# Kernel tuning notes

Measured on AMD Instinct MI355X. Metric: run time of the kernel, lower is better.

Reference implementation:

```python
import jax, jax.numpy as jnp
import numpy as np

# ---- static configuration (matches init_kwargs) ----
B = 32
H = 56
W = 56
C = 192
HEADS = 6
WS = 7            # window size
SHIFT = 3         # shift size (WS // 2)
MLP_HIDDEN = 768  # 4 * C
CPB = 256         # clip(56*56//16, 256, 1024)
N = WS * WS       # tokens per window
NW = (H // WS) * (W // WS)  # windows per image
EPS = 1e-5

# ---- static tables (Swin V2 continuous relative position bias) ----
# log-spaced relative coords table: [(2*WS-1)^2, 2]
_r = np.arange(-(WS - 1), WS, dtype=np.float32)
_tab = np.stack(np.meshgrid(_r, _r, indexing='ij'), axis=-1)  # [2WS-1, 2WS-1, 2]
_tab = _tab / (WS - 1) * 8.0  # pretrained_window_size=0 -> use window_size-1
_tab = np.sign(_tab) * np.log2(np.abs(_tab) + 1.0) / np.log2(8.0)
REL_TABLE = jnp.asarray(_tab.reshape(-1, 2))

# relative position index: [N, N] into the (2WS-1)^2 table
_coords = np.stack(np.meshgrid(np.arange(WS), np.arange(WS), indexing='ij'))
_cf = _coords.reshape(2, -1)
_rel = (_cf[:, :, None] - _cf[:, None, :]).transpose(1, 2, 0).astype(np.int64)
_rel[..., 0] += WS - 1
_rel[..., 1] += WS - 1
_rel[..., 0] *= 2 * WS - 1
REL_INDEX = jnp.asarray(_rel.sum(-1))

# shifted-window attention mask: [NW, N, N] with 0 / -100
_img = np.zeros((H, W), dtype=np.float32)
_sl = [slice(0, -WS), slice(-WS, -SHIFT), slice(-SHIFT, None)]
_cnt = 0
for _hs in _sl:
    for _ws in _sl:
        _img[_hs, _ws] = _cnt
        _cnt += 1
_mw = _img.reshape(H // WS, WS, W // WS, WS).transpose(0, 2, 1, 3).reshape(-1, N)
_am = _mw[:, None, :] - _mw[:, :, None]
ATTN_MASK = jnp.asarray(np.where(_am != 0, -100.0, 0.0).astype(np.float32))


def _layer_norm(x, g, b):
    mu = jnp.mean(x, axis=-1, keepdims=True)
    var = jnp.mean(jnp.square(x - mu), axis=-1, keepdims=True)
    return (x - mu) * jax.lax.rsqrt(var + EPS) * g + b


def setup_inputs() -> dict:
    key = jax.random.key(0)
    ks = jax.random.split(key, 10)
    def n(k, shape, s=0.02):
        return jax.random.normal(k, shape, jnp.float32) * s
    return {
        'x': jax.random.normal(ks[0], (B, H * W, C), jnp.float32),
        'qkv_w': n(ks[1], (3 * C, C)),
        'q_bias': jnp.zeros((C,), jnp.float32),
        'v_bias': jnp.zeros((C,), jnp.float32),
        'logit_scale': jnp.full((HEADS, 1, 1), jnp.log(10.0), jnp.float32),
        'cpb_w1': n(ks[2], (CPB, 2)),
        'cpb_b1': jnp.zeros((CPB,), jnp.float32),
        'cpb_w2': n(ks[3], (HEADS, CPB)),
        'proj_w': n(ks[4], (C, C)),
        'proj_b': jnp.zeros((C,), jnp.float32),
        'norm1_g': jnp.ones((C,), jnp.float32),
        'norm1_b': jnp.zeros((C,), jnp.float32),
        'norm2_g': jnp.ones((C,), jnp.float32),
        'norm2_b': jnp.zeros((C,), jnp.float32),
        'fc1_w': n(ks[5], (MLP_HIDDEN, C)),
        'fc1_b': jnp.zeros((MLP_HIDDEN,), jnp.float32),
        'fc2_w': n(ks[6], (C, MLP_HIDDEN)),
        'fc2_b': jnp.zeros((C,), jnp.float32),
    }


def reference(x, qkv_w, q_bias, v_bias, logit_scale, cpb_w1, cpb_b1, cpb_w2,
              proj_w, proj_b, norm1_g, norm1_b, norm2_g, norm2_b,
              fc1_w, fc1_b, fc2_w, fc2_b):
    b = x.shape[0]
    hd = C // HEADS
    shortcut = x

    # cyclic shift + window partition -> [b*NW, N, C]
    xi = jnp.roll(x.reshape(b, H, W, C), (-SHIFT, -SHIFT), axis=(1, 2))
    xw = xi.reshape(b, H // WS, WS, W // WS, WS, C)
    xw = xw.transpose(0, 1, 3, 2, 4, 5).reshape(-1, N, C)

    # qkv projection (k has no bias, per Swin V2)
    qkv_bias = jnp.concatenate([q_bias, jnp.zeros_like(q_bias), v_bias])
    qkv = (xw @ qkv_w.T + qkv_bias).reshape(-1, N, 3, HEADS, hd)
    qkv = qkv.transpose(2, 0, 3, 1, 4)  # [3, bw, heads, N, hd]
    q, k, v = qkv[0], qkv[1], qkv[2]

    # cosine attention with learned logit scale
    q = q / jnp.maximum(jnp.linalg.norm(q, axis=-1, keepdims=True), 1e-12)
    k = k / jnp.maximum(jnp.linalg.norm(k, axis=-1, keepdims=True), 1e-12)
    scale = jnp.exp(jnp.minimum(logit_scale, jnp.log(100.0)))  # [heads,1,1]
    attn = jnp.einsum('bhnd,bhmd->bhnm', q, k) * scale

    # continuous relative position bias via tiny MLP
    tab = jax.nn.relu(REL_TABLE @ cpb_w1.T + cpb_b1) @ cpb_w2.T  # [(2WS-1)^2, heads]
    rpb = 16.0 * jax.nn.sigmoid(tab[REL_INDEX])                  # [N, N, heads]
    attn = attn + rpb.transpose(2, 0, 1)[None]

    # shifted-window mask + softmax
    attn = attn.reshape(-1, NW, HEADS, N, N) + ATTN_MASK[None, :, None]
    attn = jax.nn.softmax(attn.reshape(-1, HEADS, N, N), axis=-1)

    out = jnp.einsum('bhnm,bhmd->bhnd', attn, v)
    out = out.transpose(0, 2, 1, 3).reshape(-1, N, C) @ proj_w.T + proj_b

    # window reverse + reverse shift
    xr = out.reshape(b, H // WS, W // WS, WS, WS, C)
    xr = xr.transpose(0, 1, 3, 2, 4, 5).reshape(b, H, W, C)
    xr = jnp.roll(xr, (SHIFT, SHIFT), axis=(1, 2)).reshape(b, H * W, C)

    # post-norm residual (Swin V2 style)
    x1 = shortcut + _layer_norm(xr, norm1_g, norm1_b)
    hmid = jax.nn.silu(x1 @ fc1_w.T + fc1_b) @ fc2_w.T + fc2_b
    return x1 + _layer_norm(hmid, norm2_g, norm2_b)
```

## Files before the change

kernel.cpp:

```cpp
#include <hip/hip_runtime.h>


typedef unsigned short ushort_t;
using f32x4  = __attribute__((ext_vector_type(4))) float;
using short8 = __attribute__((ext_vector_type(8))) short;
union LD16 { short8 v; ushort4 h[2]; };

__device__ __forceinline__ ushort_t f2bf(float f) {
  union { float f; unsigned u; } v; v.f = f;
  unsigned r = v.u + 0x7fffu + ((v.u >> 16) & 1u);
  return (ushort_t)(r >> 16);
}
__device__ __forceinline__ float bf2f(ushort_t u) {
  union { unsigned u; float f; } v; v.u = ((unsigned)u) << 16;
  return v.f;
}

__device__ __forceinline__ int img_pos(int m) {
  int win = m / 49, n = m - win * 49;
  int b = win >> 6, wi = win & 63;
  int nd = n / 7, nm = n - nd * 7;
  int hs = (wi >> 3) * 7 + nd;
  int ws = (wi & 7) * 7 + nm;
  int h = hs + 3; if (h >= 56) h -= 56;
  int w = ws + 3; if (w >= 56) w -= 56;
  return b * 3136 + h * 56 + w;
}

__device__ __forceinline__ int region3(int a) { return a < 49 ? 0 : (a < 53 ? 1 : 2); }

__global__ void cvt_kernel(const float* __restrict__ in, ushort_t* __restrict__ out, int n) {
  int i = blockIdx.x * 256 + threadIdx.x;
  if (i < n) out[i] = f2bf(in[i]);
}

__global__ __launch_bounds__(256) void gather_cvt_kernel(
    const float* __restrict__ x, ushort_t* __restrict__ xw) {
  int i8 = blockIdx.x * 256 + threadIdx.x;
  int m = i8 / 24, c8 = (i8 - m * 24) * 8;
  const float* p = x + (size_t)img_pos(m) * 192 + c8;
  float4 a = *(const float4*)p, b = *(const float4*)(p + 4);
  ushort_t* q = xw + (size_t)m * 192 + c8;
  *(ushort4*)q       = make_ushort4(f2bf(a.x), f2bf(a.y), f2bf(a.z), f2bf(a.w));
  *(ushort4*)(q + 4) = make_ushort4(f2bf(b.x), f2bf(b.y), f2bf(b.z), f2bf(b.w));
}

__global__ __launch_bounds__(256) void cpb_kernel(
    const float* __restrict__ w1, const float* __restrict__ b1,
    const float* __restrict__ w2, float* __restrict__ tab_s) {
  int e = blockIdx.x;
  int t = threadIdx.x;
  int i = e / 13, j = e - 13 * (e / 13);
  auto cval = [](int a) -> float {
    float r = (a - 6) * (8.0f / 6.0f);
    float v = log2f(fabsf(r) + 1.f) * (1.f / 3.f);
    return r < 0.f ? -v : v;
  };
  float ci = cval(i), cj = cval(j);
  float h = fmaxf(ci * w1[2 * t] + cj * w1[2 * t + 1] + b1[t], 0.f);
  __shared__ float red[256];
  for (int head = 0; head < 6; ++head) {
    red[t] = h * w2[head * 256 + t];
    __syncthreads();
    for (int st = 128; st > 0; st >>= 1) {
      if (t < st) red[t] += red[t + st];
      __syncthreads();
    }
    if (t == 0) tab_s[head * 169 + e] = 16.f / (1.f + __expf(-red[0]));
    __syncthreads();
  }
}

template<int KTOT, int MODE>
__global__ __launch_bounds__(512, 4) void gemm_n192(
    const ushort_t* __restrict__ Ab, const ushort_t* __restrict__ W,
    const float* __restrict__ b0, const float* __restrict__ b1,
    ushort_t* __restrict__ out, int NTOT) {
  __shared__ ushort_t Al[128][40];
  __shared__ ushort_t Bl[192][40];
  int t = threadIdx.x;
  int m0 = blockIdx.x * 128, n0 = blockIdx.y * 192;
  int lane = t & 63, wid = t >> 6;
  int wm = wid >> 1, wn = wid & 1;
  int lr = lane & 15, lg = lane >> 4;

  bool stager = (t < 256);
  int arow = (t & 255) >> 1, akoff = (t & 1) << 4;
  const ushort_t* Arowp = Ab + (size_t)(m0 + arow) * KTOT + akoff;
  int colA = akoff ? 4 : 0;
  int bn = (t & 255) >> 2, cB = t & 3;
  const ushort_t* Browp  = W + (size_t)(n0 + bn) * KTOT + (cB << 3);
  const ushort_t* Browp2 = W + (size_t)(n0 + 64 + bn) * KTOT + (cB << 3);
  const ushort_t* Browp3 = W + (size_t)(n0 + 128 + bn) * KTOT + (cB << 3);
  int colB = ((cB & 1) << 4) | ((cB >> 1) << 2);

  f32x4 acc[2][6];
#pragma unroll
  for (int a = 0; a < 2; ++a)
#pragma unroll
    for (int b = 0; b < 6; ++b) acc[a][b] = (f32x4){0.f, 0.f, 0.f, 0.f};

  LD16 A01, A23, B0, B1, B2;
  auto LOADREGS = [&](int kt) {
    A01.v = *(const short8*)(Arowp + kt);
    A23.v = *(const short8*)(Arowp + kt + 8);
    B0.v  = *(const short8*)(Browp + kt);
    B1.v  = *(const short8*)(Browp2 + kt);
    B2.v  = *(const short8*)(Browp3 + kt);
  };

  const int NT = KTOT / 32;
  if (stager) LOADREGS(0);
  for (int it = 0; it < NT; ++it) {
    if (stager) {
      ushort_t* Ar = &Al[arow][0];
      *(ushort4*)(Ar + colA +  0) = A01.h[0];
      *(ushort4*)(Ar + colA +  8) = A01.h[1];
      *(ushort4*)(Ar + colA + 16) = A23.h[0];
      *(ushort4*)(Ar + colA + 24) = A23.h[1];
      ushort_t* Br0 = &Bl[bn][0];
      *(ushort4*)(Br0 + colB + 0) = B0.h[0];
      *(ushort4*)(Br0 + colB + 8) = B0.h[1];
      ushort_t* Br1 = &Bl[64 + bn][0];
      *(ushort4*)(Br1 + colB + 0) = B1.h[0];
      *(ushort4*)(Br1 + colB + 8) = B1.h[1];
      ushort_t* Br2 = &Bl[128 + bn][0];
      *(ushort4*)(Br2 + colB + 0) = B2.h[0];
      *(ushort4*)(Br2 + colB + 8) = B2.h[1];
    }
    __syncthreads();
    if (stager && it + 1 < NT) LOADREGS((it + 1) * 32);
    short8 af[2], bfv[6];
#pragma unroll
    for (int fm = 0; fm < 2; ++fm)
      af[fm] = *(const short8*)&Al[wm * 32 + fm * 16 + lr][lg * 8];
#pragma unroll
    for (int fn = 0; fn < 6; ++fn)
      bfv[fn] = *(const short8*)&Bl[wn * 96 + fn * 16 + lr][lg * 8];
#pragma unroll
    for (int fm = 0; fm < 2; ++fm)
#pragma unroll
      for (int fn = 0; fn < 6; ++fn)
        acc[fm][fn] = __builtin_amdgcn_mfma_f32_16x16x32_bf16(af[fm], bfv[fn], acc[fm][fn], 0, 0, 0);
    if (it + 1 < NT) __syncthreads();
  }
#pragma unroll
  for (int fm = 0; fm < 2; ++fm) {
#pragma unroll
    for (int fn = 0; fn < 6; ++fn) {
      int col = n0 + wn * 96 + fn * 16 + lr;
      float bias;
      if (MODE == 0) bias = (col < 192) ? b0[col] : ((col < 384) ? 0.f : b1[col - 384]);
      else           bias = b0[col];
#pragma unroll
      for (int r = 0; r < 4; ++r) {
        int row = m0 + wm * 32 + fm * 16 + lg * 4 + r;
        float v = acc[fm][fn][r] + bias;
        if (MODE == 1) v = v / (1.f + __expf(-v));
        out[(size_t)row * NTOT + col] = f2bf(v);
      }
    }
  }
}

template<int KTOT, int MODE>
__global__ __launch_bounds__(512, 4) void gemm_ln512(
    const ushort_t* __restrict__ Ab, const ushort_t* __restrict__ W,
    const float* __restrict__ bias, const float* __restrict__ gamma,
    const float* __restrict__ beta, const float* __restrict__ residf,
    const ushort_t* __restrict__ residb, ushort_t* __restrict__ outb,
    float* __restrict__ outf) {
  __shared__ ushort_t Al[128][40];
  __shared__ ushort_t Bl[192][40];
  int t = threadIdx.x;
  int m0 = blockIdx.x * 128;
  int lane = t & 63, wid = t >> 6;
  int wm = wid >> 1, wn = wid & 1;
  int lr = lane & 15, lg = lane >> 4;

  bool stager = (t < 256);
  int arow = (t & 255) >> 1, akoff = (t & 1) << 4;
  const ushort_t* Arowp = Ab + (size_t)(m0 + arow) * KTOT + akoff;
  int colA = akoff ? 4 : 0;
  int bn = (t & 255) >> 2, cB = t & 3;
  const ushort_t* Browp  = W + (size_t)(bn) * KTOT + (cB << 3);
  const ushort_t* Browp2 = W + (size_t)(64 + bn) * KTOT + (cB << 3);
  const ushort_t* Browp3 = W + (size_t)(128 + bn) * KTOT + (cB << 3);
  int colB = ((cB & 1) << 4) | ((cB >> 1) << 2);

  f32x4 acc[2][6];
#pragma unroll
  for (int a = 0; a < 2; ++a)
#pragma unroll
    for (int b = 0; b < 6; ++b) acc[a][b] = (f32x4){0.f, 0.f, 0.f, 0.f};

  LD16 A01, A23, B0, B1, B2;
  auto LOADREGS = [&](int kt) {
    A01.v = *(const short8*)(Arowp + kt);
    A23.v = *(const short8*)(Arowp + kt + 8);
    B0.v  = *(const short8*)(Browp + kt);
    B1.v  = *(const short8*)(Browp2 + kt);
    B2.v  = *(const short8*)(Browp3 + kt);
  };

  const int NT = KTOT / 32;
  if (stager) LOADREGS(0);
  for (int it = 0; it < NT; ++it) {
    if (stager) {
      ushort_t* Ar = &Al[arow][0];
      *(ushort4*)(Ar + colA +  0) = A01.h[0];
      *(ushort4*)(Ar + colA +  8) = A01.h[1];
      *(ushort4*)(Ar + colA + 16) = A23.h[0];
      *(ushort4*)(Ar + colA + 24) = A23.h[1];
      ushort_t* Br0 = &Bl[bn][0];
      *(ushort4*)(Br0 + colB + 0) = B0.h[0];
      *(ushort4*)(Br0 + colB + 8) = B0.h[1];
      ushort_t* Br1 = &Bl[64 + bn][0];
      *(ushort4*)(Br1 + colB + 0) = B1.h[0];
      *(ushort4*)(Br1 + colB + 8) = B1.h[1];
      ushort_t* Br2 = &Bl[128 + bn][0];
      *(ushort4*)(Br2 + colB + 0) = B2.h[0];
      *(ushort4*)(Br2 + colB + 8) = B2.h[1];
    }
    __syncthreads();
    if (stager && it + 1 < NT) LOADREGS((it + 1) * 32);
    short8 af[2], bfv[6];
#pragma unroll
    for (int fm = 0; fm < 2; ++fm)
      af[fm] = *(const short8*)&Al[wm * 32 + fm * 16 + lr][lg * 8];
#pragma unroll
    for (int fn = 0; fn < 6; ++fn)
      bfv[fn] = *(const short8*)&Bl[wn * 96 + fn * 16 + lr][lg * 8];
#pragma unroll
    for (int fm = 0; fm < 2; ++fm)
#pragma unroll
      for (int fn = 0; fn < 6; ++fn)
        acc[fm][fn] = __builtin_amdgcn_mfma_f32_16x16x32_bf16(af[fm], bfv[fn], acc[fm][fn], 0, 0, 0);
    __syncthreads();
  }

  float* part = (float*)&Bl[0][0];
#pragma unroll
  for (int fm = 0; fm < 2; ++fm) {
#pragma unroll
    for (int r = 0; r < 4; ++r) {
      float s1 = 0.f, s2 = 0.f;
#pragma unroll
      for (int fn = 0; fn < 6; ++fn) {
        int col = wn * 96 + fn * 16 + lr;
        float v = acc[fm][fn][r] + bias[col];
        acc[fm][fn][r] = v;
        s1 += v; s2 += v * v;
      }
#pragma unroll
      for (int off = 1; off < 16; off <<= 1) {
        s1 += __shfl_xor(s1, off);
        s2 += __shfl_xor(s2, off);
      }
      if (lr == 0) {
        int lrow = wm * 32 + fm * 16 + lg * 4 + r;
        part[(wn * 128 + lrow) * 2 + 0] = s1;
        part[(wn * 128 + lrow) * 2 + 1] = s2;
      }
    }
  }
  __syncthreads();
#pragma unroll
  for (int fm = 0; fm < 2; ++fm) {
#pragma unroll
    for (int r = 0; r < 4; ++r) {
      int lrow = wm * 32 + fm * 16 + lg * 4 + r;
      float s1 = part[lrow * 2 + 0] + part[(128 + lrow) * 2 + 0];
      float s2 = part[lrow * 2 + 1] + part[(128 + lrow) * 2 + 1];
      float mean = s1 * (1.f / 192.f);
      float var  = s2 * (1.f / 192.f) - mean * mean;
      float rstd = rsqrtf(fmaxf(var, 0.f) + 1e-5f);
      int rg = m0 + lrow;
      size_t og = (MODE == 0 ? (size_t)img_pos(rg) : (size_t)rg) * 192;
#pragma unroll
      for (int fn = 0; fn < 6; ++fn) {
        int col = wn * 96 + fn * 16 + lr;
        float l = (acc[fm][fn][r] - mean) * rstd * gamma[col] + beta[col];
        if (MODE == 0) outb[og + col] = f2bf(residf[og + col] + l);
        else           outf[og + col] = bf2f(residb[og + col]) + l;
      }
    }
  }
}

__global__ __launch_bounds__(256) void attn_kernel(
    const ushort_t* __restrict__ qkv, const float* __restrict__ logit_scale,
    const float* __restrict__ tab_s, ushort_t* __restrict__ attn_out) {
  __shared__ ushort_t qs[64][40];
  __shared__ ushort_t ksl[64][40];
  __shared__ ushort_t vsl[32][80];
  __shared__ ushort_t ps[64][80];
  __shared__ float tab_l[169];
  int win = blockIdx.x, head = blockIdx.y;
  int t = threadIdx.x;
  int wi = win & 63;
  int wh0 = (wi >> 3) * 7, ww0 = (wi & 7) * 7;
  size_t base = (size_t)win * 49 * 576 + head * 32;

  for (int u = t; u < 169; u += 256) tab_l[u] = tab_s[head * 169 + u];

  for (int u = t; u < 240; u += 256) {
    int arr = u / 120, v = u - arr * 120;
    int r = 49 + (v >> 3), c4 = (v & 7) << 2;
    ushort_t* p = arr ? &ksl[r][c4] : &qs[r][c4];
    *(ushort4*)p = make_ushort4(0, 0, 0, 0);
  }

  for (int u = t; u < 2048; u += 256) {
    int key = u >> 5, d = u & 31;
    ushort_t val = 0;
    if (key < 49) val = qkv[base + (size_t)key * 576 + 384 + d];
    int kk = key & 31;
    int pc = ((key >> 5) << 5) + 8 * ((kk >> 2) & 3) + 4 * (kk >> 4) + (kk & 3);
    vsl[d][pc] = val;
  }

  float scale = __expf(fminf(logit_scale[head], 4.605170186f));

  if (t < 196) {
    int r = t >> 2, c = t & 3;
    const ushort_t* qp = qkv + base + (size_t)r * 576 + c * 8;
    ushort4 qa = *(const ushort4*)qp,         qb = *(const ushort4*)(qp + 4);
    ushort4 ka = *(const ushort4*)(qp + 192), kb = *(const ushort4*)(qp + 196);
    float qf[8] = {bf2f(qa.x), bf2f(qa.y), bf2f(qa.z), bf2f(qa.w),
                   bf2f(qb.x), bf2f(qb.y), bf2f(qb.z), bf2f(qb.w)};
    float kf[8] = {bf2f(ka.x), bf2f(ka.y), bf2f(ka.z), bf2f(ka.w),
                   bf2f(kb.x), bf2f(kb.y), bf2f(kb.z), bf2f(kb.w)};
    float sq = 0.f, sk = 0.f;
#pragma unroll
    for (int d = 0; d < 8; ++d) { sq += qf[d] * qf[d]; sk += kf[d] * kf[d]; }
    sq += __shfl_xor(sq, 1); sq += __shfl_xor(sq, 2);
    sk += __shfl_xor(sk, 1); sk += __shfl_xor(sk, 2);
    float rq = scale / fmaxf(sqrtf(sq), 1e-12f);
    float rk = 1.f   / fmaxf(sqrtf(sk), 1e-12f);
    int c0 = ((c & 1) << 4) | ((c >> 1) << 2);
    ushort_t* qd = &qs[r][c0];
    *(ushort4*)(qd + 0) = make_ushort4(f2bf(qf[0]*rq), f2bf(qf[1]*rq), f2bf(qf[2]*rq), f2bf(qf[3]*rq));
    *(ushort4*)(qd + 8) = make_ushort4(f2bf(qf[4]*rq), f2bf(qf[5]*rq), f2bf(qf[6]*rq), f2bf(qf[7]*rq));
    ushort_t* kd = &ksl[r][c0];
    *(ushort4*)(kd + 0) = make_ushort4(f2bf(kf[0]*rk), f2bf(kf[1]*rk), f2bf(kf[2]*rk), f2bf(kf[3]*rk));
    *(ushort4*)(kd + 8) = make_ushort4(f2bf(kf[4]*rk), f2bf(kf[5]*rk), f2bf(kf[6]*rk), f2bf(kf[7]*rk));
  }
  __syncthreads();

  int lane = t & 63, w = t >> 6;
  int lr = lane & 15, lg = lane >> 4;

  short8 aq = *(const short8*)&qs[w * 16 + lr][lg * 8];
  f32x4 acc[4];
#pragma unroll
  for (int fn = 0; fn < 4; ++fn) {
    acc[fn] = (f32x4){0.f, 0.f, 0.f, 0.f};
    short8 bk = *(const short8*)&ksl[fn * 16 + lr][lg * 8];
    acc[fn] = __builtin_amdgcn_mfma_f32_16x16x32_bf16(aq, bk, acc[fn], 0, 0, 0);
  }

  float rsum[4];
#pragma unroll
  for (int r = 0; r < 4; ++r) {
    int row = w * 16 + lg * 4 + r;
    int rd = (row * 9363) >> 16, rm = row - 7 * rd;
    int gr = region3(wh0 + rd) * 3 + region3(ww0 + rm);
    bool rv = row < 49;
    float sv[4];
#pragma unroll
    for (int fn = 0; fn < 4; ++fn) {
      int col = fn * 16 + lr;
      int jd = (col * 9363) >> 16, jm = col - 7 * jd;
      int gj = region3(wh0 + jd) * 3 + region3(ww0 + jm);
      bool cv = rv && (col < 49);
      int idx = cv ? (rd - jd + 6) * 13 + (rm - jm + 6) : 0;
      float s = acc[fn][r] + tab_l[idx] + (gr == gj ? 0.f : -100.f);
      sv[fn] = cv ? s : -1e30f;
    }
    float m = fmaxf(fmaxf(sv[0], sv[1]), fmaxf(sv[2], sv[3]));
#pragma unroll
    for (int o = 1; o < 16; o <<= 1) m = fmaxf(m, __shfl_xor(m, o));
    float sum = 0.f;
#pragma unroll
    for (int fn = 0; fn < 4; ++fn) {
      float e = __expf(sv[fn] - m);
      sum += e;
      int pc = ((fn >> 1) << 5) + 8 * (lr >> 2) + ((fn & 1) << 2) + (lr & 3);
      ps[row][pc] = f2bf(e);
    }
#pragma unroll
    for (int o = 1; o < 16; o <<= 1) sum += __shfl_xor(sum, o);
    rsum[r] = 1.f / sum;
  }
  __syncthreads();

  short8 ap0 = *(const short8*)&ps[w * 16 + lr][lg * 8];
  short8 ap1 = *(const short8*)&ps[w * 16 + lr][32 + lg * 8];
  f32x4 o2[2];
#pragma unroll
  for (int f = 0; f < 2; ++f) {
    o2[f] = (f32x4){0.f, 0.f, 0.f, 0.f};
    short8 bv0 = *(const short8*)&vsl[f * 16 + lr][lg * 8];
    short8 bv1 = *(const short8*)&vsl[f * 16 + lr][32 + lg * 8];
    o2[f] = __builtin_amdgcn_mfma_f32_16x16x32_bf16(ap0, bv0, o2[f], 0, 0, 0);
    o2[f] = __builtin_amdgcn_mfma_f32_16x16x32_bf16(ap1, bv1, o2[f], 0, 0, 0);
  }
#pragma unroll
  for (int f = 0; f < 2; ++f) {
#pragma unroll
    for (int r = 0; r < 4; ++r) {
      int row = w * 16 + lg * 4 + r;
      if (row < 49)
        attn_out[((size_t)win * 49 + row) * 192 + head * 32 + f * 16 + lr] =
            f2bf(o2[f][r] * rsum[r]);
    }
  }
}

extern "C" void kernel_launch(void* const* d_in, const int* in_sizes, int n_in,
                              void* d_out, int out_size, void* d_ws, size_t ws_size,
                              hipStream_t stream) {
  (void)in_sizes; (void)n_in; (void)out_size; (void)ws_size;
  const float* x    = (const float*)d_in[0];
  const float* qkvw = (const float*)d_in[1];
  const float* qb   = (const float*)d_in[2];
  const float* vb   = (const float*)d_in[3];
  const float* ls   = (const float*)d_in[4];
  const float* cw1  = (const float*)d_in[5];
  const float* cb1  = (const float*)d_in[6];
  const float* cw2  = (const float*)d_in[7];
  const float* pw   = (const float*)d_in[8];
  const float* pb   = (const float*)d_in[9];
  const float* n1g  = (const float*)d_in[10];
  const float* n1b  = (const float*)d_in[11];
  const float* n2g  = (const float*)d_in[12];
  const float* n2b  = (const float*)d_in[13];
  const float* f1w  = (const float*)d_in[14];
  const float* f1b  = (const float*)d_in[15];
  const float* f2w  = (const float*)d_in[16];
  const float* f2b  = (const float*)d_in[17];
  float* out = (float*)d_out;

  char* ws = (char*)d_ws;
  ushort_t* wq_bf = (ushort_t*)ws;
  ushort_t* wp_bf = wq_bf + 110592;
  ushort_t* w1_bf = wp_bf + 36864;
  ushort_t* w2_bf = w1_bf + 147456;
  float*    tab_s = (float*)(w2_bf + 147456);
  const size_t OFF_BIG = 1 << 20;
  ushort_t* qkv_out = (ushort_t*)(ws + OFF_BIG);
  ushort_t* xw_bf   = (ushort_t*)(ws + OFF_BIG + 115605504);
  ushort_t* attn_o  = (ushort_t*)(ws + OFF_BIG + 115605504);
  ushort_t* x1_bf   = (ushort_t*)(ws + OFF_BIG + 154140672);
  ushort_t* hmid    = (ushort_t*)(ws + OFF_BIG);

  cvt_kernel<<<(110592 + 255) / 256, 256, 0, stream>>>(qkvw, wq_bf, 110592);
  cvt_kernel<<<(36864  + 255) / 256, 256, 0, stream>>>(pw,   wp_bf, 36864);
  cvt_kernel<<<(147456 + 255) / 256, 256, 0, stream>>>(f1w,  w1_bf, 147456);
  cvt_kernel<<<(147456 + 255) / 256, 256, 0, stream>>>(f2w,  w2_bf, 147456);
  cpb_kernel<<<169, 256, 0, stream>>>(cw1, cb1, cw2, tab_s);
  gather_cvt_kernel<<<9408, 256, 0, stream>>>(x, xw_bf);

  gemm_n192<192, 0><<<dim3(784, 3), 512, 0, stream>>>(xw_bf, wq_bf, qb, vb, qkv_out, 576);
  attn_kernel<<<dim3(2048, 6), 256, 0, stream>>>(qkv_out, ls, tab_s, attn_o);
  gemm_ln512<192, 0><<<784, 512, 0, stream>>>(attn_o, wp_bf, pb, n1g, n1b, x, nullptr, x1_bf, nullptr);
  gemm_n192<192, 1><<<dim3(784, 4), 512, 0, stream>>>(x1_bf, w1_bf, f1b, nullptr, hmid, 768);
  gemm_ln512<768, 1><<<784, 512, 0, stream>>>(hmid, w2_bf, f2b, n2g, n2b, nullptr, x1_bf, nullptr, out);
}
```

Before: 413.1 us.

## Split projection GEMM from LayerNorm residual into separate kernels

The fused projection GEMM plus LayerNorm epilogue is replaced by a plain GEMM that writes the projection output in place over the attention buffer. A new wave-per-row kernel then does LayerNorm, the shifted-image scatter and the residual add. The fc2 LayerNorm kernel is specialised and drops one redundant barrier on the last K iteration. This removes the cross-wave partial-sum exchange and scattered epilogue from the GEMM, at the cost of an extra full read and write of the activation tensor, plus in-place aliasing that relies on each block owning its rows.

```diff
diff --git a/kernel.cpp b/kernel.cpp
--- a/kernel.cpp
+++ b/kernel.cpp
@@ -75,7 +75,7 @@
 __global__ __launch_bounds__(512, 4) void gemm_n192(
     const ushort_t* __restrict__ Ab, const ushort_t* __restrict__ W,
     const float* __restrict__ b0, const float* __restrict__ b1,
-    ushort_t* __restrict__ out, int NTOT) {
+    ushort_t* out, int NTOT) {
   __shared__ ushort_t Al[128][40];
   __shared__ ushort_t Bl[192][40];
   int t = threadIdx.x;
@@ -163,13 +163,12 @@
   }
 }
 
-template<int KTOT, int MODE>
-__global__ __launch_bounds__(512, 4) void gemm_ln512(
+__global__ __launch_bounds__(512, 4) void gemm_ln_fc2(
     const ushort_t* __restrict__ Ab, const ushort_t* __restrict__ W,
     const float* __restrict__ bias, const float* __restrict__ gamma,
-    const float* __restrict__ beta, const float* __restrict__ residf,
-    const ushort_t* __restrict__ residb, ushort_t* __restrict__ outb,
+    const float* __restrict__ beta, const ushort_t* __restrict__ residb,
     float* __restrict__ outf) {
+  const int KTOT = 768;
   __shared__ ushort_t Al[128][40];
   __shared__ ushort_t Bl[192][40];
   int t = threadIdx.x;
@@ -236,8 +235,9 @@
 #pragma unroll
       for (int fn = 0; fn < 6; ++fn)
         acc[fm][fn] = __builtin_amdgcn_mfma_f32_16x16x32_bf16(af[fm], bfv[fn], acc[fm][fn], 0, 0, 0);
-    __syncthreads();
-  }
+    if (it + 1 < NT) __syncthreads();
+  }
+  __syncthreads();
 
   float* part = (float*)&Bl[0][0];
 #pragma unroll
@@ -275,17 +275,42 @@
       float mean = s1 * (1.f / 192.f);
       float var  = s2 * (1.f / 192.f) - mean * mean;
       float rstd = rsqrtf(fmaxf(var, 0.f) + 1e-5f);
-      int rg = m0 + lrow;
-      size_t og = (MODE == 0 ? (size_t)img_pos(rg) : (size_t)rg) * 192;
+      size_t og = (size_t)(m0 + lrow) * 192;
 #pragma unroll
       for (int fn = 0; fn < 6; ++fn) {
         int col = wn * 96 + fn * 16 + lr;
         float l = (acc[fm][fn][r] - mean) * rstd * gamma[col] + beta[col];
-        if (MODE == 0) outb[og + col] = f2bf(residf[og + col] + l);
-        else           outf[og + col] = bf2f(residb[og + col]) + l;
+        outf[og + col] = bf2f(residb[og + col]) + l;
       }
     }
   }
+}
+
+__global__ __launch_bounds__(256) void ln_resid_kernel(
+    const ushort_t* __restrict__ pre, const float* __restrict__ residf,
+    const float* __restrict__ gamma, const float* __restrict__ beta,
+    ushort_t* __restrict__ outb) {
+  int m = (blockIdx.x * 256 + threadIdx.x) >> 6;
+  int lane = threadIdx.x & 63;
+  const ushort_t* p = pre + (size_t)m * 192;
+  float v0 = bf2f(p[lane]), v1 = bf2f(p[lane + 64]), v2 = bf2f(p[lane + 128]);
+  float s1 = v0 + v1 + v2;
+  float s2 = v0 * v0 + v1 * v1 + v2 * v2;
+#pragma unroll
+  for (int o = 1; o < 64; o <<= 1) {
+    s1 += __shfl_xor(s1, o);
+    s2 += __shfl_xor(s2, o);
+  }
+  float mean = s1 * (1.f / 192.f);
+  float var  = s2 * (1.f / 192.f) - mean * mean;
+  float rstd = rsqrtf(fmaxf(var, 0.f) + 1e-5f);
+  float l0 = (v0 - mean) * rstd * gamma[lane]       + beta[lane];
+  float l1 = (v1 - mean) * rstd * gamma[lane + 64]  + beta[lane + 64];
+  float l2 = (v2 - mean) * rstd * gamma[lane + 128] + beta[lane + 128];
+  size_t og = (size_t)img_pos(m) * 192;
+  outb[og + lane]       = f2bf(residf[og + lane]       + l0);
+  outb[og + lane + 64]  = f2bf(residf[og + lane + 64]  + l1);
+  outb[og + lane + 128] = f2bf(residf[og + lane + 128] + l2);
 }
 
 __global__ __launch_bounds__(256) void attn_kernel(
@@ -464,7 +489,8 @@
 
   gemm_n192<192, 0><<<dim3(784, 3), 512, 0, stream>>>(xw_bf, wq_bf, qb, vb, qkv_out, 576);
   attn_kernel<<<dim3(2048, 6), 256, 0, stream>>>(qkv_out, ls, tab_s, attn_o);
-  gemm_ln512<192, 0><<<784, 512, 0, stream>>>(attn_o, wp_bf, pb, n1g, n1b, x, nullptr, x1_bf, nullptr);
+  gemm_n192<192, 2><<<dim3(784, 1), 512, 0, stream>>>(attn_o, wp_bf, pb, nullptr, attn_o, 192);
+  ln_resid_kernel<<<25088, 256, 0, stream>>>(attn_o, x, n1g, n1b, x1_bf);
   gemm_n192<192, 1><<<dim3(784, 4), 512, 0, stream>>>(x1_bf, w1_bf, f1b, nullptr, hmid, 768);
-  gemm_ln512<768, 1><<<784, 512, 0, stream>>>(hmid, w2_bf, f2b, n2g, n2b, nullptr, x1_bf, nullptr, out);
-}
+  gemm_ln_fc2<<<784, 512, 0, stream>>>(hmid, w2_bf, f2b, n2g, n2b, x1_bf, out);
+}
```

Measured after the change: 396.8 us. 3.9% less time.
